# Kernel optimization log

Measured on AMD Instinct MI355X. Metric: run time of the kernel, lower is better.

The kernel has to match this reference:

```python
import jax, jax.numpy as jnp
import numpy as np

N = 50000
E = 1600000


def _gcn_norm(edge_index, num_nodes):
    # PyG gcn_norm with add_self_loops=True, edge_weight=1:
    # append self loops, deg = in-degree over dst (col), norm = d_src^-1/2 * d_dst^-1/2
    loops = jnp.arange(num_nodes, dtype=edge_index.dtype)
    src = jnp.concatenate([edge_index[0], loops])
    dst = jnp.concatenate([edge_index[1], loops])
    deg = jax.ops.segment_sum(jnp.ones_like(dst, dtype=jnp.float32), dst,
                              num_segments=num_nodes)
    dinv = jnp.where(deg > 0, jax.lax.rsqrt(deg), 0.0)
    norm = dinv[src] * dinv[dst]  # [E+N]
    return src, dst, norm


def _gcn_layer(x, W, b, src, dst, norm, num_nodes):
    h = x @ W                                  # [N, out]
    msg = h[src] * norm[:, None]               # gather + scale, [E+N, out]
    out = jax.ops.segment_sum(msg, dst, num_segments=num_nodes)
    return out + b


def setup_inputs() -> dict:
    key = jax.random.key(0)
    ks = jax.random.split(key, 10)
    d_in, d_h, d_out = 128, 128, 64
    s = lambda d: 1.0 / np.sqrt(d)
    return {
        "x": jax.random.normal(ks[0], (N, d_in), dtype=jnp.float32),
        "edge_index": jax.random.randint(ks[1], (2, E), 0, N, dtype=jnp.int64),
        "W1": jax.random.normal(ks[2], (d_in, d_h), dtype=jnp.float32) * s(d_in),
        "b1": jnp.zeros((d_h,), dtype=jnp.float32),
        "W2": jax.random.normal(ks[3], (d_h, d_h), dtype=jnp.float32) * s(d_h),
        "b2": jnp.zeros((d_h,), dtype=jnp.float32),
        "W3": jax.random.normal(ks[4], (d_h, d_h), dtype=jnp.float32) * s(d_h),
        "b3": jnp.zeros((d_h,), dtype=jnp.float32),
        "W4": jax.random.normal(ks[5], (d_h, d_out), dtype=jnp.float32) * s(d_h),
        "b4": jnp.zeros((d_out,), dtype=jnp.float32),
    }


def reference(x, edge_index, W1, b1, W2, b2, W3, b3, W4, b4):
    src, dst, norm = _gcn_norm(edge_index, N)
    h = jax.nn.relu(_gcn_layer(x, W1, b1, src, dst, norm, N))
    h = jax.nn.relu(_gcn_layer(h, W2, b2, src, dst, norm, N))
    h = jax.nn.relu(_gcn_layer(h, W3, b3, src, dst, norm, N))
    h = _gcn_layer(h, W4, b4, src, dst, norm, N)
    return h
```

## Files before the change

### kernel.cpp

```cpp
#include <hip/hip_runtime.h>
#include <hip/hip_fp16.h>

constexpr int K_DIM = 128;

typedef _Float16 f16x8 __attribute__((ext_vector_type(8)));
typedef float f32x4 __attribute__((ext_vector_type(4)));

#define GLOAD16(g, l) __builtin_amdgcn_global_load_lds( \
    (const __attribute__((address_space(1))) void*)(g), \
    (__attribute__((address_space(3))) void*)(l), 16, 0, 0)

__global__ __launch_bounds__(256) void bcount_k(const int* __restrict__ dst, int E,
    int* __restrict__ bcount, int NBr) {
  __shared__ int h[256];
  const int tid = threadIdx.x;
  h[tid] = 0;
  __syncthreads();
  for (int t = blockIdx.x * 256 + tid; t < E; t += gridDim.x * 256)
    atomicAdd(&h[dst[t] >> 8], 1);
  __syncthreads();
  if (tid < NBr && h[tid]) atomicAdd(&bcount[tid], h[tid]);
}

__global__ __launch_bounds__(256) void bscan_k(const int* __restrict__ bcount,
    int* __restrict__ bstart, int* __restrict__ bcursor, int NBr) {
  __shared__ int sh[256];
  const int t = threadIdx.x;
  sh[t] = (t < NBr) ? bcount[t] : 0;
  __syncthreads();
  for (int off = 1; off < 256; off <<= 1) {
    int w = (t >= off) ? sh[t - off] : 0;
    __syncthreads();
    sh[t] += w;
    __syncthreads();
  }
  if (t < NBr) {
    int ex = t ? sh[t - 1] : 0;
    bstart[t] = ex;
    bcursor[t] = ex;
  }
  if (t == NBr - 1) bstart[NBr] = sh[t];
}

__global__ __launch_bounds__(256) void bscatter_k(const int* __restrict__ ei, int E,
    int* __restrict__ bcursor, unsigned* __restrict__ brec, int NBr) {
  __shared__ int h[256];
  __shared__ int base[256];
  const int tid = threadIdx.x;
  h[tid] = 0;
  __syncthreads();
  const int chunk = (E + gridDim.x - 1) / gridDim.x;
  const int s = blockIdx.x * chunk;
  const int e = min(E, s + chunk);
  for (int t = s + tid; t < e; t += 256) atomicAdd(&h[ei[E + t] >> 8], 1);
  __syncthreads();
  if (tid < NBr && h[tid]) base[tid] = atomicAdd(&bcursor[tid], h[tid]);
  __syncthreads();
  for (int t = s + tid; t < e; t += 256) {
    int src = ei[t];
    int d = ei[E + t];
    int bk = d >> 8;
    int p = atomicAdd(&base[bk], 1);
    brec[p] = ((unsigned)src << 8) | (unsigned)(d & 255);
  }
}

__global__ __launch_bounds__(256) void bcsr_k(const unsigned* __restrict__ brec,
    const int* __restrict__ bstart, int n, int E,
    int* __restrict__ rowptr, int* __restrict__ colidx, float* __restrict__ dinv) {
  __shared__ int s_deg[256];
  __shared__ int s_cur[256];
  __shared__ int s_lrp[257];
  const int b = blockIdx.x, tid = threadIdx.x;
  const int node0 = b << 8;
  const int LC = min(256, n - node0);
  const int rs = bstart[b], cnt = bstart[b + 1] - rs;

  s_deg[tid] = (tid < LC) ? 1 : 0;
  __syncthreads();
  for (int i = tid; i < cnt; i += 256) atomicAdd(&s_deg[brec[rs + i] & 255], 1);
  __syncthreads();
  s_cur[tid] = s_deg[tid];
  __syncthreads();
  for (int off = 1; off < 256; off <<= 1) {
    int w = (tid >= off) ? s_cur[tid - off] : 0;
    __syncthreads();
    s_cur[tid] += w;
    __syncthreads();
  }
  s_lrp[tid + 1] = s_cur[tid];
  if (tid == 0) s_lrp[0] = 0;
  __syncthreads();

  const int gbase = rs + node0;
  if (tid < LC) {
    int p = s_lrp[tid];
    colidx[gbase + p] = node0 + tid;
    s_cur[tid] = p + 1;
    rowptr[node0 + tid] = gbase + p;
    dinv[node0 + tid] = rsqrtf((float)(s_lrp[tid + 1] - p));
  }
  __syncthreads();
  for (int i = tid; i < cnt; i += 256) {
    unsigned r = brec[rs + i];
    int p = atomicAdd(&s_cur[r & 255], 1);
    colidx[gbase + p] = (int)(r >> 8);
  }
  if (b == (int)gridDim.x - 1 && tid == 0) rowptr[n] = E + n;
}

__global__ __launch_bounds__(256) void prep_k(const float* __restrict__ x,
    __half* __restrict__ z, long total4,
    const float* __restrict__ W1, const float* __restrict__ W2,
    const float* __restrict__ W3, const float* __restrict__ W4,
    __half* __restrict__ wth, __half* __restrict__ wtl) {
  long t = (long)blockIdx.x * 256 + threadIdx.x;
  if (t < total4) {
    float4 v = reinterpret_cast<const float4*>(x)[t];
    union { __half2 h[2]; uint2 u; } uu;
    uu.h[0] = __floats2half2_rn(v.x, v.y);
    uu.h[1] = __floats2half2_rn(v.z, v.w);
    reinterpret_cast<uint2*>(z)[t] = uu.u;
  }
  if (t < 57344) {
    int id = (int)t;
    const float* W;
    int nout, base, rem;
    if (id < 49152) {
      int l = id / 16384;
      W = (l == 0) ? W1 : (l == 1) ? W2 : W3;
      nout = 128;
      base = l * 16384;
      rem = id - base;
    } else {
      W = W4;
      nout = 64;
      base = 49152;
      rem = id - base;
    }
    int k = rem / nout, c = rem % nout;
    float w = W[k * nout + c];
    __half hi = __float2half_rn(w);
    __half lo = __float2half_rn(w - __half2float(hi));
    wth[base + c * 128 + k] = hi;
    wtl[base + c * 128 + k] = lo;
  }
}

template<int NOUT>
__global__ __launch_bounds__(256) void gemm_mfma_k(
    const __half* __restrict__ Z,
    const __half* __restrict__ Wh, const __half* __restrict__ Wl,
    const float* __restrict__ dinv, __half* __restrict__ H, int n) {
  constexpr int NT = NOUT / 32;
  __shared__ __half Az[32][32];
  __shared__ __half Bh[NOUT][32];
  __shared__ __half Bl[NOUT][32];
  const int tid = threadIdx.x;
  const int lane = tid & 63;
  const int w = tid >> 6;
  const int r16 = lane & 15;
  const int kb = lane >> 4;
  const int row0 = blockIdx.x * 32;
  const int rh = w & 1;
  const int ch = w >> 1;
  const int sw = (r16 + (r16 >> 2)) & 3;

  f32x4 acc[NT];
  #pragma unroll
  for (int t = 0; t < NT; ++t)
    #pragma unroll
    for (int q = 0; q < 4; ++q) acc[t][q] = 0.f;

  char* AzB = (char*)&Az[0][0];
  char* BhB = (char*)&Bh[0][0];
  char* BlB = (char*)&Bl[0][0];

  for (int kc = 0; kc < 128; kc += 32) {
    __syncthreads();
    if (w < 2) {
      int r = tid >> 2;
      int q = (tid & 3) ^ ((r + (r >> 2)) & 3);
      int rc = row0 + r; rc = (rc < n) ? rc : (n - 1);
      GLOAD16(Z + (size_t)rc * 128 + kc + q * 8, AzB + w * 1024);
    }
    {
      int c = tid >> 2;
      int q = (tid & 3) ^ ((c + (c >> 2)) & 3);
      GLOAD16(Wh + (size_t)c * 128 + kc + q * 8, BhB + w * 1024);
      GLOAD16(Wl + (size_t)c * 128 + kc + q * 8, BlB + w * 1024);
      if constexpr (NOUT == 128) {
        int i1 = tid + 256;
        int c1 = i1 >> 2;
        int q1 = (i1 & 3) ^ ((c1 + (c1 >> 2)) & 3);
        GLOAD16(Wh + (size_t)c1 * 128 + kc + q1 * 8, BhB + 4096 + w * 1024);
        GLOAD16(Wl + (size_t)c1 * 128 + kc + q1 * 8, BlB + 4096 + w * 1024);
      }
    }
    __syncthreads();

    const int ao = (kb ^ sw) * 8;
    f16x8 az = *(const f16x8*)&Az[rh * 16 + r16][ao];
    #pragma unroll
    for (int t = 0; t < NT; ++t) {
      int c = ch * (NOUT / 2) + t * 16 + r16;
      f16x8 bh = *(const f16x8*)&Bh[c][ao];
      f16x8 bl = *(const f16x8*)&Bl[c][ao];
      acc[t] = __builtin_amdgcn_mfma_f32_16x16x32_f16(az, bh, acc[t], 0, 0, 0);
      acc[t] = __builtin_amdgcn_mfma_f32_16x16x32_f16(az, bl, acc[t], 0, 0, 0);
    }
  }

  #pragma unroll
  for (int q = 0; q < 4; ++q) {
    int grow = row0 + rh * 16 + kb * 4 + q;
    if (grow < n) {
      float dsc = dinv[grow];
      #pragma unroll
      for (int t = 0; t < NT; ++t) {
        int col = ch * (NOUT / 2) + t * 16 + r16;
        H[(size_t)grow * NOUT + col] = __float2half(dsc * acc[t][q]);
      }
    }
  }
}

__global__ __launch_bounds__(256) void agg128_k(const __half* __restrict__ H,
    const int* __restrict__ rowptr, const int* __restrict__ colidx,
    const float* __restrict__ dinv, const float* __restrict__ bias,
    __half* __restrict__ Z, int n) {
  const int wave = threadIdx.x >> 6;
  const int lane = threadIdx.x & 63;
  const int node = blockIdx.x * 4 + wave;
  if (node >= n) return;
  const int s = rowptr[node], e = rowptr[node + 1];
  const __half2* H2 = reinterpret_cast<const __half2*>(H);

  float ax = 0.f, ay = 0.f;
  for (int base = s; base < e; base += 64) {
    int m = e - base;
    int c = __builtin_nontemporal_load(&colidx[base + ((lane < m) ? lane : 0)]);
    int kmax = (m < 64) ? m : 64;
    int k = 0;
    for (; k + 7 < kmax; k += 8) {
      int cc[8];
      float2 hh[8];
      #pragma unroll
      for (int u = 0; u < 8; ++u) cc[u] = __shfl(c, k + u);
      #pragma unroll
      for (int u = 0; u < 8; ++u) hh[u] = __half22float2(H2[(size_t)cc[u] * 64 + lane]);
      #pragma unroll
      for (int u = 0; u < 8; ++u) { ax += hh[u].x; ay += hh[u].y; }
    }
    for (; k < kmax; ++k) {
      int ck = __shfl(c, k);
      float2 h = __half22float2(H2[(size_t)ck * 64 + lane]);
      ax += h.x;
      ay += h.y;
    }
  }
  float d = dinv[node];
  float2 b2 = reinterpret_cast<const float2*>(bias)[lane];
  float ox = fmaxf(fmaf(d, ax, b2.x), 0.f);
  float oy = fmaxf(fmaf(d, ay, b2.y), 0.f);
  __half2 hv = __floats2half2_rn(ox, oy);
  unsigned vv = *reinterpret_cast<unsigned*>(&hv);
  __builtin_nontemporal_store(vv, reinterpret_cast<unsigned*>(Z) + (size_t)node * 64 + lane);
}

__global__ __launch_bounds__(256) void agg64_k(const __half* __restrict__ H,
    const int* __restrict__ rowptr, const int* __restrict__ colidx,
    const float* __restrict__ dinv, const float* __restrict__ bias,
    float* __restrict__ out, int n) {
  const int wave = threadIdx.x >> 6;
  const int lane = threadIdx.x & 63;
  const int node = blockIdx.x * 4 + wave;
  if (node >= n) return;
  const int s = rowptr[node], e = rowptr[node + 1];

  float a0 = 0.f;
  for (int base = s; base < e; base += 64) {
    int m = e - base;
    int c = __builtin_nontemporal_load(&colidx[base + ((lane < m) ? lane : 0)]);
    int kmax = (m < 64) ? m : 64;
    int k = 0;
    for (; k + 7 < kmax; k += 8) {
      int cc[8];
      float hh[8];
      #pragma unroll
      for (int u = 0; u < 8; ++u) cc[u] = __shfl(c, k + u);
      #pragma unroll
      for (int u = 0; u < 8; ++u) hh[u] = __half2float(H[(size_t)cc[u] * 64 + lane]);
      #pragma unroll
      for (int u = 0; u < 8; ++u) a0 += hh[u];
    }
    for (; k < kmax; ++k) {
      int ck = __shfl(c, k);
      a0 += __half2float(H[(size_t)ck * 64 + lane]);
    }
  }
  float o = fmaf(dinv[node], a0, bias[lane]);
  __builtin_nontemporal_store(o, &out[(size_t)node * 64 + lane]);
}

extern "C" void kernel_launch(void* const* d_in, const int* in_sizes, int n_in,
                              void* d_out, int out_size, void* d_ws, size_t ws_size,
                              hipStream_t stream) {
  const int n = in_sizes[0] / K_DIM;
  const int E = in_sizes[1] / 2;
  const int NBr = (n + 255) >> 8;

  const float* x  = (const float*)d_in[0];
  const int*   ei = (const int*)d_in[1];
  const float* W1 = (const float*)d_in[2];
  const float* b1 = (const float*)d_in[3];
  const float* W2 = (const float*)d_in[4];
  const float* b2 = (const float*)d_in[5];
  const float* W3 = (const float*)d_in[6];
  const float* b3 = (const float*)d_in[7];
  const float* W4 = (const float*)d_in[8];
  const float* b4 = (const float*)d_in[9];
  float* out = (float*)d_out;

  char* ws = (char*)d_ws;
  size_t off = 0;
  auto alloc = [&](size_t bytes) -> void* {
    void* p = ws + off;
    off += (bytes + 255) & ~(size_t)255;
    return p;
  };
  int*      bcount  = (int*)     alloc(256 * 4);
  int*      bstart  = (int*)     alloc(257 * 4);
  int*      bcursor = (int*)     alloc(256 * 4);
  unsigned* brec    = (unsigned*)alloc((size_t)E * 4);
  int*      rowptr  = (int*)     alloc((size_t)(n + 1) * 4);
  int*      colidx  = (int*)     alloc((size_t)(E + n) * 4);
  float*    dinv    = (float*)   alloc((size_t)n * 4);
  __half*   Z       = (__half*)  alloc((size_t)n * 128 * 2);
  __half*   hH      = (__half*)  alloc((size_t)n * 128 * 2);
  __half*   wth     = (__half*)  alloc((size_t)57344 * 2);
  __half*   wtl     = (__half*)  alloc((size_t)57344 * 2);

  hipMemsetAsync(bcount, 0, 256 * 4, stream);
  bcount_k<<<512, 256, 0, stream>>>(ei + E, E, bcount, NBr);
  bscan_k<<<1, 256, 0, stream>>>(bcount, bstart, bcursor, NBr);
  bscatter_k<<<256, 256, 0, stream>>>(ei, E, bcursor, brec, NBr);
  bcsr_k<<<NBr, 256, 0, stream>>>(brec, bstart, n, E, rowptr, colidx, dinv);

  const long total4 = (long)n * 32;
  prep_k<<<(int)((total4 + 255) / 256), 256, 0, stream>>>(x, Z, total4,
                                                          W1, W2, W3, W4, wth, wtl);

  const int gb = (n + 31) / 32;
  const int ab = (n + 3) / 4;

  gemm_mfma_k<128><<<gb, 256, 0, stream>>>(Z, wth, wtl, dinv, hH, n);
  agg128_k<<<ab, 256, 0, stream>>>(hH, rowptr, colidx, dinv, b1, Z, n);
  gemm_mfma_k<128><<<gb, 256, 0, stream>>>(Z, wth + 16384, wtl + 16384, dinv, hH, n);
  agg128_k<<<ab, 256, 0, stream>>>(hH, rowptr, colidx, dinv, b2, Z, n);
  gemm_mfma_k<128><<<gb, 256, 0, stream>>>(Z, wth + 32768, wtl + 32768, dinv, hH, n);
  agg128_k<<<ab, 256, 0, stream>>>(hH, rowptr, colidx, dinv, b3, Z, n);
  gemm_mfma_k<64><<<gb, 256, 0, stream>>>(Z, wth + 49152, wtl + 49152, dinv, hH, n);
  agg64_k<<<ab, 256, 0, stream>>>(hH, rowptr, colidx, dinv, b4, out, n);
}
```

Measured before the change: 319.3 us.

## Tile aggregation by source-node ranges and shrink column indices to 16 bits

The CSR build now buckets each destination's neighbours by source tile (8192-node ranges) and records per-node, per-tile offsets. Column indices are stored as 16-bit values. The aggregation kernels use a fixed grid in which each wave owns 7 strided nodes and walks the source tiles in order. All waves therefore gather from the same slice of H at roughly the same time, which is meant to improve L2 hit rate and cut index bandwidth. In exchange, each node's edges are split into many tiny segments with extra loop and tail overhead, and the code assumes n < 65536 and at most 7 tiles.

```diff
diff --git a/kernel.cpp b/kernel.cpp
--- a/kernel.cpp
+++ b/kernel.cpp
@@ -67,44 +67,68 @@
 
 __global__ __launch_bounds__(256) void bcsr_k(const unsigned* __restrict__ brec,
     const int* __restrict__ bstart, int n, int E,
-    int* __restrict__ rowptr, int* __restrict__ colidx, float* __restrict__ dinv) {
-  __shared__ int s_deg[256];
-  __shared__ int s_cur[256];
+    int* __restrict__ rowptr, unsigned short* __restrict__ colidx,
+    float* __restrict__ dinv, int* __restrict__ tptr) {
+  __shared__ int s_cnt[256 * 8];
+  __shared__ int s_cur[256 * 8];
+  __shared__ int s_scan[256];
   __shared__ int s_lrp[257];
   const int b = blockIdx.x, tid = threadIdx.x;
   const int node0 = b << 8;
   const int LC = min(256, n - node0);
   const int rs = bstart[b], cnt = bstart[b + 1] - rs;
 
-  s_deg[tid] = (tid < LC) ? 1 : 0;
-  __syncthreads();
-  for (int i = tid; i < cnt; i += 256) atomicAdd(&s_deg[brec[rs + i] & 255], 1);
-  __syncthreads();
-  s_cur[tid] = s_deg[tid];
+  #pragma unroll
+  for (int t = 0; t < 8; ++t) s_cnt[tid * 8 + t] = 0;
+  __syncthreads();
+  for (int i = tid; i < cnt; i += 256) {
+    unsigned r = brec[rs + i];
+    atomicAdd(&s_cnt[(r & 255) * 8 + (int)((r >> 8) >> 13)], 1);
+  }
+  if (tid < LC) atomicAdd(&s_cnt[tid * 8 + ((node0 + tid) >> 13)], 1);
+  __syncthreads();
+
+  int deg = 0;
+  #pragma unroll
+  for (int t = 0; t < 8; ++t) deg += s_cnt[tid * 8 + t];
+  s_scan[tid] = deg;
   __syncthreads();
   for (int off = 1; off < 256; off <<= 1) {
-    int w = (tid >= off) ? s_cur[tid - off] : 0;
-    __syncthreads();
-    s_cur[tid] += w;
-    __syncthreads();
-  }
-  s_lrp[tid + 1] = s_cur[tid];
+    int w = (tid >= off) ? s_scan[tid - off] : 0;
+    __syncthreads();
+    s_scan[tid] += w;
+    __syncthreads();
+  }
+  s_lrp[tid + 1] = s_scan[tid];
   if (tid == 0) s_lrp[0] = 0;
   __syncthreads();
 
   const int gbase = rs + node0;
   if (tid < LC) {
-    int p = s_lrp[tid];
-    colidx[gbase + p] = node0 + tid;
-    s_cur[tid] = p + 1;
-    rowptr[node0 + tid] = gbase + p;
-    dinv[node0 + tid] = rsqrtf((float)(s_lrp[tid + 1] - p));
-  }
-  __syncthreads();
+    int node = node0 + tid;
+    int gstart = gbase + s_lrp[tid];
+    rowptr[node] = gstart;
+    dinv[node] = rsqrtf((float)(s_lrp[tid + 1] - s_lrp[tid]));
+    int off = gstart;
+    #pragma unroll
+    for (int t = 0; t < 8; ++t) {
+      tptr[(size_t)node * 8 + t] = off;
+      s_cur[tid * 8 + t] = off;
+      off += s_cnt[tid * 8 + t];
+    }
+  }
+  __syncthreads();
+  if (tid < LC) {
+    int node = node0 + tid;
+    int p = atomicAdd(&s_cur[tid * 8 + (node >> 13)], 1);
+    colidx[p] = (unsigned short)node;
+  }
   for (int i = tid; i < cnt; i += 256) {
     unsigned r = brec[rs + i];
-    int p = atomicAdd(&s_cur[r & 255], 1);
-    colidx[gbase + p] = (int)(r >> 8);
+    int d = r & 255;
+    int src = (int)(r >> 8);
+    int p = atomicAdd(&s_cur[d * 8 + (src >> 13)], 1);
+    colidx[p] = (unsigned short)src;
   }
   if (b == (int)gridDim.x - 1 && tid == 0) rowptr[n] = E + n;
 }
@@ -226,81 +250,118 @@
 }
 
 __global__ __launch_bounds__(256) void agg128_k(const __half* __restrict__ H,
-    const int* __restrict__ rowptr, const int* __restrict__ colidx,
+    const unsigned short* __restrict__ colidx, const int* __restrict__ tptr,
     const float* __restrict__ dinv, const float* __restrict__ bias,
-    __half* __restrict__ Z, int n) {
+    __half* __restrict__ Z, int n, int ntile) {
   const int wave = threadIdx.x >> 6;
   const int lane = threadIdx.x & 63;
-  const int node = blockIdx.x * 4 + wave;
-  if (node >= n) return;
-  const int s = rowptr[node], e = rowptr[node + 1];
+  const int W = blockIdx.x * 4 + wave;
   const __half2* H2 = reinterpret_cast<const __half2*>(H);
-
-  float ax = 0.f, ay = 0.f;
-  for (int base = s; base < e; base += 64) {
-    int m = e - base;
-    int c = __builtin_nontemporal_load(&colidx[base + ((lane < m) ? lane : 0)]);
-    int kmax = (m < 64) ? m : 64;
-    int k = 0;
-    for (; k + 7 < kmax; k += 8) {
-      int cc[8];
-      float2 hh[8];
-      #pragma unroll
-      for (int u = 0; u < 8; ++u) cc[u] = __shfl(c, k + u);
-      #pragma unroll
-      for (int u = 0; u < 8; ++u) hh[u] = __half22float2(H2[(size_t)cc[u] * 64 + lane]);
-      #pragma unroll
-      for (int u = 0; u < 8; ++u) { ax += hh[u].x; ay += hh[u].y; }
-    }
-    for (; k < kmax; ++k) {
-      int ck = __shfl(c, k);
-      float2 h = __half22float2(H2[(size_t)ck * 64 + lane]);
-      ax += h.x;
-      ay += h.y;
-    }
-  }
-  float d = dinv[node];
+  constexpr int NPW = 7;
+
+  float ax[NPW], ay[NPW];
+  #pragma unroll
+  for (int i = 0; i < NPW; ++i) { ax[i] = 0.f; ay[i] = 0.f; }
+
+  for (int t = 0; t < ntile; ++t) {
+    #pragma unroll
+    for (int i = 0; i < NPW; ++i) {
+      int nd = W + i * 8192;
+      if (nd < n) {
+        int st = tptr[(size_t)nd * 8 + t];
+        int en = tptr[(size_t)nd * 8 + t + 1];
+        for (int base = st; base < en; base += 64) {
+          int m = en - base;
+          int c = (int)colidx[base + ((lane < m) ? lane : 0)];
+          int kmax = (m < 64) ? m : 64;
+          int k = 0;
+          for (; k + 3 < kmax; k += 4) {
+            int cc[4]; float2 hh[4];
+            #pragma unroll
+            for (int u = 0; u < 4; ++u) cc[u] = __shfl(c, k + u);
+            #pragma unroll
+            for (int u = 0; u < 4; ++u) hh[u] = __half22float2(H2[(size_t)cc[u] * 64 + lane]);
+            #pragma unroll
+            for (int u = 0; u < 4; ++u) { ax[i] += hh[u].x; ay[i] += hh[u].y; }
+          }
+          for (; k < kmax; ++k) {
+            int ck = __shfl(c, k);
+            float2 h = __half22float2(H2[(size_t)ck * 64 + lane]);
+            ax[i] += h.x;
+            ay[i] += h.y;
+          }
+        }
+      }
+    }
+  }
+
   float2 b2 = reinterpret_cast<const float2*>(bias)[lane];
-  float ox = fmaxf(fmaf(d, ax, b2.x), 0.f);
-  float oy = fmaxf(fmaf(d, ay, b2.y), 0.f);
-  __half2 hv = __floats2half2_rn(ox, oy);
-  unsigned vv = *reinterpret_cast<unsigned*>(&hv);
-  __builtin_nontemporal_store(vv, reinterpret_cast<unsigned*>(Z) + (size_t)node * 64 + lane);
+  #pragma unroll
+  for (int i = 0; i < NPW; ++i) {
+    int nd = W + i * 8192;
+    if (nd < n) {
+      float d = dinv[nd];
+      float ox = fmaxf(fmaf(d, ax[i], b2.x), 0.f);
+      float oy = fmaxf(fmaf(d, ay[i], b2.y), 0.f);
+      __half2 hv = __floats2half2_rn(ox, oy);
+      unsigned vv = *reinterpret_cast<unsigned*>(&hv);
+      __builtin_nontemporal_store(vv, reinterpret_cast<unsigned*>(Z) + (size_t)nd * 64 + lane);
+    }
+  }
 }
 
 __global__ __launch_bounds__(256) void agg64_k(const __half* __restrict__ H,
-    const int* __restrict__ rowptr, const int* __restrict__ colidx,
+    const unsigned short* __restrict__ colidx, const int* __restrict__ tptr,
     const float* __restrict__ dinv, const float* __restrict__ bias,
-    float* __restrict__ out, int n) {
+    float* __restrict__ out, int n, int ntile) {
   const int wave = threadIdx.x >> 6;
   const int lane = threadIdx.x & 63;
-  const int node = blockIdx.x * 4 + wave;
-  if (node >= n) return;
-  const int s = rowptr[node], e = rowptr[node + 1];
-
-  float a0 = 0.f;
-  for (int base = s; base < e; base += 64) {
-    int m = e - base;
-    int c = __builtin_nontemporal_load(&colidx[base + ((lane < m) ? lane : 0)]);
-    int kmax = (m < 64) ? m : 64;
-    int k = 0;
-    for (; k + 7 < kmax; k += 8) {
-      int cc[8];
-      float hh[8];
-      #pragma unroll
-      for (int u = 0; u < 8; ++u) cc[u] = __shfl(c, k + u);
-      #pragma unroll
-      for (int u = 0; u < 8; ++u) hh[u] = __half2float(H[(size_t)cc[u] * 64 + lane]);
-      #pragma unroll
-      for (int u = 0; u < 8; ++u) a0 += hh[u];
-    }
-    for (; k < kmax; ++k) {
-      int ck = __shfl(c, k);
-      a0 += __half2float(H[(size_t)ck * 64 + lane]);
-    }
-  }
-  float o = fmaf(dinv[node], a0, bias[lane]);
-  __builtin_nontemporal_store(o, &out[(size_t)node * 64 + lane]);
+  const int W = blockIdx.x * 4 + wave;
+  constexpr int NPW = 7;
+
+  float a0[NPW];
+  #pragma unroll
+  for (int i = 0; i < NPW; ++i) a0[i] = 0.f;
+
+  for (int t = 0; t < ntile; ++t) {
+    #pragma unroll
+    for (int i = 0; i < NPW; ++i) {
+      int nd = W + i * 8192;
+      if (nd < n) {
+        int st = tptr[(size_t)nd * 8 + t];
+        int en = tptr[(size_t)nd * 8 + t + 1];
+        for (int base = st; base < en; base += 64) {
+          int m = en - base;
+          int c = (int)colidx[base + ((lane < m) ? lane : 0)];
+          int kmax = (m < 64) ? m : 64;
+          int k = 0;
+          for (; k + 3 < kmax; k += 4) {
+            int cc[4]; float hh[4];
+            #pragma unroll
+            for (int u = 0; u < 4; ++u) cc[u] = __shfl(c, k + u);
+            #pragma unroll
+            for (int u = 0; u < 4; ++u) hh[u] = __half2float(H[(size_t)cc[u] * 64 + lane]);
+            #pragma unroll
+            for (int u = 0; u < 4; ++u) a0[i] += hh[u];
+          }
+          for (; k < kmax; ++k) {
+            int ck = __shfl(c, k);
+            a0[i] += __half2float(H[(size_t)ck * 64 + lane]);
+          }
+        }
+      }
+    }
+  }
+
+  float bv = bias[lane];
+  #pragma unroll
+  for (int i = 0; i < NPW; ++i) {
+    int nd = W + i * 8192;
+    if (nd < n) {
+      float o = fmaf(dinv[nd], a0[i], bv);
+      __builtin_nontemporal_store(o, &out[(size_t)nd * 64 + lane]);
+    }
+  }
 }
 
 extern "C" void kernel_launch(void* const* d_in, const int* in_sizes, int n_in,
@@ -309,6 +370,7 @@
   const int n = in_sizes[0] / K_DIM;
   const int E = in_sizes[1] / 2;
   const int NBr = (n + 255) >> 8;
+  const int ntile = ((n - 1) >> 13) + 1;
 
   const float* x  = (const float*)d_in[0];
   const int*   ei = (const int*)d_in[1];
@@ -334,7 +396,8 @@
   int*      bcursor = (int*)     alloc(256 * 4);
   unsigned* brec    = (unsigned*)alloc((size_t)E * 4);
   int*      rowptr  = (int*)     alloc((size_t)(n + 1) * 4);
-  int*      colidx  = (int*)     alloc((size_t)(E + n) * 4);
+  unsigned short* colidx = (unsigned short*)alloc((size_t)(E + n) * 2);
+  int*      tptr    = (int*)     alloc((size_t)n * 8 * 4);
   float*    dinv    = (float*)   alloc((size_t)n * 4);
   __half*   Z       = (__half*)  alloc((size_t)n * 128 * 2);
   __half*   hH      = (__half*)  alloc((size_t)n * 128 * 2);
@@ -345,21 +408,21 @@
   bcount_k<<<512, 256, 0, stream>>>(ei + E, E, bcount, NBr);
   bscan_k<<<1, 256, 0, stream>>>(bcount, bstart, bcursor, NBr);
   bscatter_k<<<256, 256, 0, stream>>>(ei, E, bcursor, brec, NBr);
-  bcsr_k<<<NBr, 256, 0, stream>>>(brec, bstart, n, E, rowptr, colidx, dinv);
+  bcsr_k<<<NBr, 256, 0, stream>>>(brec, bstart, n, E, rowptr, colidx, dinv, tptr);
 
   const long total4 = (long)n * 32;
   prep_k<<<(int)((total4 + 255) / 256), 256, 0, stream>>>(x, Z, total4,
                                                           W1, W2, W3, W4, wth, wtl);
 
   const int gb = (n + 31) / 32;
-  const int ab = (n + 3) / 4;
+  const int agb = 2048;
 
   gemm_mfma_k<128><<<gb, 256, 0, stream>>>(Z, wth, wtl, dinv, hH, n);
-  agg128_k<<<ab, 256, 0, stream>>>(hH, rowptr, colidx, dinv, b1, Z, n);
+  agg128_k<<<agb, 256, 0, stream>>>(hH, colidx, tptr, dinv, b1, Z, n, ntile);
   gemm_mfma_k<128><<<gb, 256, 0, stream>>>(Z, wth + 16384, wtl + 16384, dinv, hH, n);
-  agg128_k<<<ab, 256, 0, stream>>>(hH, rowptr, colidx, dinv, b2, Z, n);
+  agg128_k<<<agb, 256, 0, stream>>>(hH, colidx, tptr, dinv, b2, Z, n, ntile);
   gemm_mfma_k<128><<<gb, 256, 0, stream>>>(Z, wth + 32768, wtl + 32768, dinv, hH, n);
-  agg128_k<<<ab, 256, 0, stream>>>(hH, rowptr, colidx, dinv, b3, Z, n);
+  agg128_k<<<agb, 256, 0, stream>>>(hH, colidx, tptr, dinv, b3, Z, n, ntile);
   gemm_mfma_k<64><<<gb, 256, 0, stream>>>(Z, wth + 49152, wtl + 49152, dinv, hH, n);
-  agg64_k<<<ab, 256, 0, stream>>>(hH, rowptr, colidx, dinv, b4, out, n);
-}
+  agg64_k<<<agb, 256, 0, stream>>>(hH, colidx, tptr, dinv, b4, out, n, ntile);
+}
```

After: 403.9 us. +26.5%, slower.

## Use 16-bit column indices and split each row's neighbors by source half

Applied to the files above, without the earlier changes.

The CSR build now stores column indices as 16-bit values and buckets each row's neighbors into two groups, sources below and above n/2. A two-entry-per-node pointer array replaces rowptr. The aggregation kernels walk the low-source segment before the high-source segment. The aim is to halve index bandwidth and to make feature gathers hit a smaller working set of H in cache, at the cost of an extra atomic bucket and an assumption that node ids fit in 16 bits.

```diff
diff --git a/kernel.cpp b/kernel.cpp
--- a/kernel.cpp
+++ b/kernel.cpp
@@ -66,47 +66,65 @@
 }
 
 __global__ __launch_bounds__(256) void bcsr_k(const unsigned* __restrict__ brec,
-    const int* __restrict__ bstart, int n, int E,
-    int* __restrict__ rowptr, int* __restrict__ colidx, float* __restrict__ dinv) {
-  __shared__ int s_deg[256];
-  __shared__ int s_cur[256];
+    const int* __restrict__ bstart, int n, int E, int half,
+    unsigned short* __restrict__ colidx, float* __restrict__ dinv,
+    int* __restrict__ tptr) {
+  __shared__ int s_cnt[256 * 2];
+  __shared__ int s_cur[256 * 2];
+  __shared__ int s_scan[256];
   __shared__ int s_lrp[257];
   const int b = blockIdx.x, tid = threadIdx.x;
   const int node0 = b << 8;
   const int LC = min(256, n - node0);
   const int rs = bstart[b], cnt = bstart[b + 1] - rs;
 
-  s_deg[tid] = (tid < LC) ? 1 : 0;
-  __syncthreads();
-  for (int i = tid; i < cnt; i += 256) atomicAdd(&s_deg[brec[rs + i] & 255], 1);
-  __syncthreads();
-  s_cur[tid] = s_deg[tid];
+  s_cnt[tid * 2] = 0;
+  s_cnt[tid * 2 + 1] = 0;
+  __syncthreads();
+  for (int i = tid; i < cnt; i += 256) {
+    unsigned r = brec[rs + i];
+    int src = (int)(r >> 8);
+    atomicAdd(&s_cnt[(r & 255) * 2 + (src >= half)], 1);
+  }
+  if (tid < LC) atomicAdd(&s_cnt[tid * 2 + ((node0 + tid) >= half)], 1);
+  __syncthreads();
+
+  s_scan[tid] = s_cnt[tid * 2] + s_cnt[tid * 2 + 1];
   __syncthreads();
   for (int off = 1; off < 256; off <<= 1) {
-    int w = (tid >= off) ? s_cur[tid - off] : 0;
-    __syncthreads();
-    s_cur[tid] += w;
-    __syncthreads();
-  }
-  s_lrp[tid + 1] = s_cur[tid];
+    int w = (tid >= off) ? s_scan[tid - off] : 0;
+    __syncthreads();
+    s_scan[tid] += w;
+    __syncthreads();
+  }
+  s_lrp[tid + 1] = s_scan[tid];
   if (tid == 0) s_lrp[0] = 0;
   __syncthreads();
 
   const int gbase = rs + node0;
   if (tid < LC) {
-    int p = s_lrp[tid];
-    colidx[gbase + p] = node0 + tid;
-    s_cur[tid] = p + 1;
-    rowptr[node0 + tid] = gbase + p;
-    dinv[node0 + tid] = rsqrtf((float)(s_lrp[tid + 1] - p));
-  }
-  __syncthreads();
+    int node = node0 + tid;
+    int gstart = gbase + s_lrp[tid];
+    dinv[node] = rsqrtf((float)(s_lrp[tid + 1] - s_lrp[tid]));
+    tptr[(size_t)node * 2] = gstart;
+    tptr[(size_t)node * 2 + 1] = gstart + s_cnt[tid * 2];
+    s_cur[tid * 2] = gstart;
+    s_cur[tid * 2 + 1] = gstart + s_cnt[tid * 2];
+  }
+  __syncthreads();
+  if (tid < LC) {
+    int node = node0 + tid;
+    int p = atomicAdd(&s_cur[tid * 2 + (node >= half)], 1);
+    colidx[p] = (unsigned short)node;
+  }
   for (int i = tid; i < cnt; i += 256) {
     unsigned r = brec[rs + i];
-    int p = atomicAdd(&s_cur[r & 255], 1);
-    colidx[gbase + p] = (int)(r >> 8);
-  }
-  if (b == (int)gridDim.x - 1 && tid == 0) rowptr[n] = E + n;
+    int d = r & 255;
+    int src = (int)(r >> 8);
+    int p = atomicAdd(&s_cur[d * 2 + (src >= half)], 1);
+    colidx[p] = (unsigned short)src;
+  }
+  if (b == (int)gridDim.x - 1 && tid == 0) tptr[(size_t)n * 2] = E + n;
 }
 
 __global__ __launch_bounds__(256) void prep_k(const float* __restrict__ x,
@@ -226,37 +244,41 @@
 }
 
 __global__ __launch_bounds__(256) void agg128_k(const __half* __restrict__ H,
-    const int* __restrict__ rowptr, const int* __restrict__ colidx,
+    const unsigned short* __restrict__ colidx, const int* __restrict__ tptr,
     const float* __restrict__ dinv, const float* __restrict__ bias,
     __half* __restrict__ Z, int n) {
   const int wave = threadIdx.x >> 6;
   const int lane = threadIdx.x & 63;
   const int node = blockIdx.x * 4 + wave;
   if (node >= n) return;
-  const int s = rowptr[node], e = rowptr[node + 1];
   const __half2* H2 = reinterpret_cast<const __half2*>(H);
 
   float ax = 0.f, ay = 0.f;
-  for (int base = s; base < e; base += 64) {
-    int m = e - base;
-    int c = __builtin_nontemporal_load(&colidx[base + ((lane < m) ? lane : 0)]);
-    int kmax = (m < 64) ? m : 64;
-    int k = 0;
-    for (; k + 7 < kmax; k += 8) {
-      int cc[8];
-      float2 hh[8];
-      #pragma unroll
-      for (int u = 0; u < 8; ++u) cc[u] = __shfl(c, k + u);
-      #pragma unroll
-      for (int u = 0; u < 8; ++u) hh[u] = __half22float2(H2[(size_t)cc[u] * 64 + lane]);
-      #pragma unroll
-      for (int u = 0; u < 8; ++u) { ax += hh[u].x; ay += hh[u].y; }
-    }
-    for (; k < kmax; ++k) {
-      int ck = __shfl(c, k);
-      float2 h = __half22float2(H2[(size_t)ck * 64 + lane]);
-      ax += h.x;
-      ay += h.y;
+  #pragma unroll
+  for (int t = 0; t < 2; ++t) {
+    const int s = tptr[(size_t)node * 2 + t];
+    const int e = tptr[(size_t)node * 2 + t + 1];
+    for (int base = s; base < e; base += 64) {
+      int m = e - base;
+      int c = (int)__builtin_nontemporal_load(&colidx[base + ((lane < m) ? lane : 0)]);
+      int kmax = (m < 64) ? m : 64;
+      int k = 0;
+      for (; k + 7 < kmax; k += 8) {
+        int cc[8];
+        float2 hh[8];
+        #pragma unroll
+        for (int u = 0; u < 8; ++u) cc[u] = __shfl(c, k + u);
+        #pragma unroll
+        for (int u = 0; u < 8; ++u) hh[u] = __half22float2(H2[(size_t)cc[u] * 64 + lane]);
+        #pragma unroll
+        for (int u = 0; u < 8; ++u) { ax += hh[u].x; ay += hh[u].y; }
+      }
+      for (; k < kmax; ++k) {
+        int ck = __shfl(c, k);
+        float2 h = __half22float2(H2[(size_t)ck * 64 + lane]);
+        ax += h.x;
+        ay += h.y;
+      }
     }
   }
   float d = dinv[node];
@@ -269,34 +291,38 @@
 }
 
 __global__ __launch_bounds__(256) void agg64_k(const __half* __restrict__ H,
-    const int* __restrict__ rowptr, const int* __restrict__ colidx,
+    const unsigned short* __restrict__ colidx, const int* __restrict__ tptr,
     const float* __restrict__ dinv, const float* __restrict__ bias,
     float* __restrict__ out, int n) {
   const int wave = threadIdx.x >> 6;
   const int lane = threadIdx.x & 63;
   const int node = blockIdx.x * 4 + wave;
   if (node >= n) return;
-  const int s = rowptr[node], e = rowptr[node + 1];
 
   float a0 = 0.f;
-  for (int base = s; base < e; base += 64) {
-    int m = e - base;
-    int c = __builtin_nontemporal_load(&colidx[base + ((lane < m) ? lane : 0)]);
-    int kmax = (m < 64) ? m : 64;
-    int k = 0;
-    for (; k + 7 < kmax; k += 8) {
-      int cc[8];
-      float hh[8];
-      #pragma unroll
-      for (int u = 0; u < 8; ++u) cc[u] = __shfl(c, k + u);
-      #pragma unroll
-      for (int u = 0; u < 8; ++u) hh[u] = __half2float(H[(size_t)cc[u] * 64 + lane]);
-      #pragma unroll
-      for (int u = 0; u < 8; ++u) a0 += hh[u];
-    }
-    for (; k < kmax; ++k) {
-      int ck = __shfl(c, k);
-      a0 += __half2float(H[(size_t)ck * 64 + lane]);
+  #pragma unroll
+  for (int t = 0; t < 2; ++t) {
+    const int s = tptr[(size_t)node * 2 + t];
+    const int e = tptr[(size_t)node * 2 + t + 1];
+    for (int base = s; base < e; base += 64) {
+      int m = e - base;
+      int c = (int)__builtin_nontemporal_load(&colidx[base + ((lane < m) ? lane : 0)]);
+      int kmax = (m < 64) ? m : 64;
+      int k = 0;
+      for (; k + 7 < kmax; k += 8) {
+        int cc[8];
+        float hh[8];
+        #pragma unroll
+        for (int u = 0; u < 8; ++u) cc[u] = __shfl(c, k + u);
+        #pragma unroll
+        for (int u = 0; u < 8; ++u) hh[u] = __half2float(H[(size_t)cc[u] * 64 + lane]);
+        #pragma unroll
+        for (int u = 0; u < 8; ++u) a0 += hh[u];
+      }
+      for (; k < kmax; ++k) {
+        int ck = __shfl(c, k);
+        a0 += __half2float(H[(size_t)ck * 64 + lane]);
+      }
     }
   }
   float o = fmaf(dinv[node], a0, bias[lane]);
@@ -309,6 +335,7 @@
   const int n = in_sizes[0] / K_DIM;
   const int E = in_sizes[1] / 2;
   const int NBr = (n + 255) >> 8;
+  const int half = (n + 1) >> 1;
 
   const float* x  = (const float*)d_in[0];
   const int*   ei = (const int*)d_in[1];
@@ -333,8 +360,8 @@
   int*      bstart  = (int*)     alloc(257 * 4);
   int*      bcursor = (int*)     alloc(256 * 4);
   unsigned* brec    = (unsigned*)alloc((size_t)E * 4);
-  int*      rowptr  = (int*)     alloc((size_t)(n + 1) * 4);
-  int*      colidx  = (int*)     alloc((size_t)(E + n) * 4);
+  unsigned short* colidx = (unsigned short*)alloc((size_t)(E + n) * 2);
+  int*      tptr    = (int*)     alloc(((size_t)n * 2 + 1) * 4);
   float*    dinv    = (float*)   alloc((size_t)n * 4);
   __half*   Z       = (__half*)  alloc((size_t)n * 128 * 2);
   __half*   hH      = (__half*)  alloc((size_t)n * 128 * 2);
@@ -345,7 +372,7 @@
   bcount_k<<<512, 256, 0, stream>>>(ei + E, E, bcount, NBr);
   bscan_k<<<1, 256, 0, stream>>>(bcount, bstart, bcursor, NBr);
   bscatter_k<<<256, 256, 0, stream>>>(ei, E, bcursor, brec, NBr);
-  bcsr_k<<<NBr, 256, 0, stream>>>(brec, bstart, n, E, rowptr, colidx, dinv);
+  bcsr_k<<<NBr, 256, 0, stream>>>(brec, bstart, n, E, half, colidx, dinv, tptr);
 
   const long total4 = (long)n * 32;
   prep_k<<<(int)((total4 + 255) / 256), 256, 0, stream>>>(x, Z, total4,
@@ -355,11 +382,11 @@
   const int ab = (n + 3) / 4;
 
   gemm_mfma_k<128><<<gb, 256, 0, stream>>>(Z, wth, wtl, dinv, hH, n);
-  agg128_k<<<ab, 256, 0, stream>>>(hH, rowptr, colidx, dinv, b1, Z, n);
+  agg128_k<<<ab, 256, 0, stream>>>(hH, colidx, tptr, dinv, b1, Z, n);
   gemm_mfma_k<128><<<gb, 256, 0, stream>>>(Z, wth + 16384, wtl + 16384, dinv, hH, n);
-  agg128_k<<<ab, 256, 0, stream>>>(hH, rowptr, colidx, dinv, b2, Z, n);
+  agg128_k<<<ab, 256, 0, stream>>>(hH, colidx, tptr, dinv, b2, Z, n);
   gemm_mfma_k<128><<<gb, 256, 0, stream>>>(Z, wth + 32768, wtl + 32768, dinv, hH, n);
-  agg128_k<<<ab, 256, 0, stream>>>(hH, rowptr, colidx, dinv, b3, Z, n);
+  agg128_k<<<ab, 256, 0, stream>>>(hH, colidx, tptr, dinv, b3, Z, n);
   gemm_mfma_k<64><<<gb, 256, 0, stream>>>(Z, wth + 49152, wtl + 49152, dinv, hH, n);
-  agg64_k<<<ab, 256, 0, stream>>>(hH, rowptr, colidx, dinv, b4, out, n);
-}
+  agg64_k<<<ab, 256, 0, stream>>>(hH, colidx, tptr, dinv, b4, out, n);
+}
```

Measured after the change: 359.1 us. 12.5% more time.
